# Performance work log

Hardware: AMD Instinct MI355X
Metric: run time of the kernel (lower is better)

Reference implementation:

```python
import jax, jax.numpy as jnp
import numpy as np

B, N, D, H = 4, 2048, 256, 4
DH = D // H
SS = DH ** -0.25  # sqrt(scale), applied to both qk0 and qk1
EPS = 1e-5


def _split_heads(t):
    # [B, N, D] -> [B, H, N, DH]
    b, n, _ = t.shape
    return t.reshape(b, n, H, DH).transpose(0, 2, 1, 3)


def _merge_heads(t):
    # [B, H, N, DH] -> [B, N, D]
    b, h, n, dh = t.shape
    return t.transpose(0, 2, 1, 3).reshape(b, n, h * dh)


def _layernorm(x, g, b):
    mu = jnp.mean(x, axis=-1, keepdims=True)
    var = jnp.mean(jnp.square(x - mu), axis=-1, keepdims=True)
    return (x - mu) * jax.lax.rsqrt(var + EPS) * g + b


def setup_inputs() -> dict:
    key = jax.random.key(0)
    ks = jax.random.split(key, 16)
    s = 0.02
    return {
        "x0": jax.random.normal(ks[0], (B, N, D), jnp.float32),
        "x1": jax.random.normal(ks[1], (B, N, D), jnp.float32),
        # weights stored as [in, out] (y = x @ W + b), matching torch Linear math
        "Wqk": jax.random.normal(ks[2], (D, D), jnp.float32) * s,
        "bqk": jnp.zeros((D,), jnp.float32),
        "Wv": jax.random.normal(ks[3], (D, D), jnp.float32) * s,
        "bv": jnp.zeros((D,), jnp.float32),
        "Wo": jax.random.normal(ks[4], (D, D), jnp.float32) * s,
        "bo": jnp.zeros((D,), jnp.float32),
        "W1": jax.random.normal(ks[5], (2 * D, 2 * D), jnp.float32) * s,
        "b1": jnp.zeros((2 * D,), jnp.float32),
        "ln_g": jnp.ones((2 * D,), jnp.float32),
        "ln_b": jnp.zeros((2 * D,), jnp.float32),
        "W2": jax.random.normal(ks[6], (2 * D, D), jnp.float32) * s,
        "b2": jnp.zeros((D,), jnp.float32),
    }


def reference(x0, x1, Wqk, bqk, Wv, bv, Wo, bo, W1, b1, ln_g, ln_b, W2, b2):
    qk0 = _split_heads(x0 @ Wqk + bqk) * SS  # [B,H,N,DH]
    qk1 = _split_heads(x1 @ Wqk + bqk) * SS
    v0 = _split_heads(x0 @ Wv + bv)
    v1 = _split_heads(x1 @ Wv + bv)

    # single shared similarity matrix, reused for both softmax directions
    sim = jnp.einsum("bhid,bhjd->bhij", qk0, qk1)  # [B,H,N0,N1]
    attn01 = jax.nn.softmax(sim, axis=-1)                      # rows over j
    attn10 = jax.nn.softmax(jnp.swapaxes(sim, -1, -2), axis=-1)  # rows over i

    m0 = jnp.einsum("bhij,bhjd->bhid", attn01, v1)  # [B,H,N0,DH]
    m1 = jnp.einsum("bhji,bhjd->bhid", jnp.swapaxes(attn10, -1, -2), v0)

    m0 = _merge_heads(m0) @ Wo + bo  # [B,N,D]
    m1 = _merge_heads(m1) @ Wo + bo

    def ffn(x, m):
        h = jnp.concatenate([x, m], axis=-1) @ W1 + b1
        h = jax.nn.gelu(_layernorm(h, ln_g, ln_b), approximate=False)
        return x + h @ W2 + b2

    return ffn(x0, m0), ffn(x1, m1)
```

## Files before the change

### kernel.cpp

```cpp
#include <hip/hip_runtime.h>
#include <hip/hip_bf16.h>
#include <math.h>

#define DEV static __device__ __forceinline__

typedef float f32x4 __attribute__((ext_vector_type(4)));
typedef short s16x8 __attribute__((ext_vector_type(8)));
typedef unsigned short u16;
typedef unsigned int u32;
typedef u32 u32x2 __attribute__((ext_vector_type(2)));
typedef u16 u16x4 __attribute__((ext_vector_type(4)));
typedef u16 u16x8 __attribute__((ext_vector_type(8)));

#define SSCALE 0.35355339059327379f

DEV f32x4 mfma16(s16x8 a, s16x8 b, f32x4 c) {
  return __builtin_amdgcn_mfma_f32_16x16x32_bf16(a, b, c, 0, 0, 0);
}

DEV float bf2f(u16 x) { u32 u = ((u32)x) << 16; float f; __builtin_memcpy(&f, &u, 4); return f; }
DEV u16 f2bf(float x) { __hip_bfloat16 b = __float2bfloat16(x); u16 r; __builtin_memcpy(&r, &b, 2); return r; }

DEV void gload_lds16(const void* g, void* l) {
  __builtin_amdgcn_global_load_lds((const __attribute__((address_space(1))) u32*)g,
                                   (__attribute__((address_space(3))) u32*)l, 16, 0, 0);
}

__global__ __launch_bounds__(256) void k_prep(
    const float* __restrict__ x0, const float* __restrict__ x1,
    const float* __restrict__ Wqk, const float* __restrict__ Wv,
    const float* __restrict__ Wo, const float* __restrict__ W1,
    const float* __restrict__ W2, const float* __restrict__ bo,
    const float* __restrict__ b1,
    u16* __restrict__ btqkv, u16* __restrict__ btF,
    u16* __restrict__ bt2, float* __restrict__ bc, u16* __restrict__ Xb)
{
  const int blk = blockIdx.x, tid = threadIdx.x;
  if (blk < 2048) {
    int idx = blk * 2048 + tid * 8;
    const float* src = (idx < 2097152) ? (x0 + idx) : (x1 + (idx - 2097152));
    f32x4 va = *(const f32x4*)src;
    f32x4 vb = *(const f32x4*)(src + 4);
    u16x8 o;
#pragma unroll
    for (int j = 0; j < 4; ++j) { o[j] = f2bf(va[j]); o[4 + j] = f2bf(vb[j]); }
    *(u16x8*)(Xb + idx) = o;
  } else if (blk < 2144) {
    __shared__ float T[64][65];
    int tb = blk - 2048;
    const float* src; u16* dst; int sld, dld, kr0, c0, drow0;
    if (tb < 16)      { src = Wqk; dst = btqkv; sld = 256; dld = 256; drow0 = 0;
                        kr0 = (tb >> 2) * 64; c0 = (tb & 3) * 64; }
    else if (tb < 32) { tb -= 16; src = Wv; dst = btqkv; sld = 256; dld = 256; drow0 = 256;
                        kr0 = (tb >> 2) * 64; c0 = (tb & 3) * 64; }
    else if (tb < 64) { tb -= 32; src = W1; dst = btF; sld = 512; dld = 512; drow0 = 0;
                        kr0 = (tb >> 3) * 64; c0 = (tb & 7) * 64; }
    else              { tb -= 64; src = W2; dst = bt2; sld = 256; dld = 512; drow0 = 0;
                        kr0 = (tb >> 2) * 64; c0 = (tb & 3) * 64; }
    int r = tid >> 2, cq = (tid & 3) * 16;
#pragma unroll
    for (int q = 0; q < 4; ++q) {
      f32x4 v = *(const f32x4*)(src + (size_t)(kr0 + r) * sld + c0 + cq + q * 4);
#pragma unroll
      for (int e = 0; e < 4; ++e) T[r][cq + q * 4 + e] = v[e];
    }
    __syncthreads();
    int c = tid >> 2, kq = (tid & 3) * 16;
#pragma unroll
    for (int q = 0; q < 2; ++q) {
      u16x8 o;
#pragma unroll
      for (int e = 0; e < 8; ++e) o[e] = f2bf(T[kq + q * 8 + e][c]);
      *(u16x8*)(dst + (size_t)(drow0 + c0 + c) * dld + kr0 + kq + q * 8) = o;
    }
  } else if (blk < 2656) {
    int wb = blk - 2144;
    int i = wb >> 1;
    int n = (wb & 1) * 256 + tid;
    float a0 = 0.f, a1 = 0.f, a2 = 0.f, a3 = 0.f;
    for (int j = 0; j < 256; j += 4) {
      a0 = fmaf(Wo[i * 256 + j],     W1[(size_t)(256 + j) * 512 + n], a0);
      a1 = fmaf(Wo[i * 256 + j + 1], W1[(size_t)(257 + j) * 512 + n], a1);
      a2 = fmaf(Wo[i * 256 + j + 2], W1[(size_t)(258 + j) * 512 + n], a2);
      a3 = fmaf(Wo[i * 256 + j + 3], W1[(size_t)(259 + j) * 512 + n], a3);
    }
    btF[(size_t)n * 512 + 256 + i] = f2bf((a0 + a1) + (a2 + a3));
  } else {
    int n = (blk - 2656) * 256 + tid;
    float acc = b1[n];
    for (int j = 0; j < 256; ++j)
      acc = fmaf(bo[j], W1[(size_t)(256 + j) * 512 + n], acc);
    bc[n] = acc;
  }
}

template <int KD, int K1, int EPI, int BN>
__global__ __launch_bounds__(256, 2) void k_gemm(
    const u16* __restrict__ A1, const u16* __restrict__ A2,
    const u16* __restrict__ Bt,
    const float* __restrict__ bias, const float* __restrict__ bias2,
    const float* __restrict__ res0, const float* __restrict__ res1,
    u16* __restrict__ outb, u16* __restrict__ outb2,
    float* __restrict__ outf, int Ncols)
{
  constexpr int MR = (BN == 128) ? 4 : 2;
  __shared__ char lds[16384 + 2 * BN * 64];
  char* ldsA = lds;
  char* ldsB = lds + 16384;
  const int tid = threadIdx.x;
  const int lane = tid & 63;
  const int w = tid >> 6;
  const int wm = (BN == 128) ? (w >> 1) : w;
  const int wn = (BN == 128) ? (w & 1) : 0;
  const int g = lane >> 4, li = lane & 15;
  const int m0 = blockIdx.x * 128, n0 = blockIdx.y * BN;

  auto stage = [&](int buf, int t) {
    const int k0 = t * 32;
#pragma unroll
    for (int it = 0; it < 2; ++it) {
      int chunk = it * 256 + w * 64 + lane;
      int row = chunk >> 2, c = chunk & 3;
      int kc = k0 + ((c ^ ((row >> 1) & 3)) << 3);
      const u16* src = (kc < K1) ? (A1 + (size_t)(m0 + row) * K1 + kc)
                                 : (A2 + (size_t)(m0 + row) * (KD - K1) + (kc - K1));
      gload_lds16(src, ldsA + buf * 8192 + (it * 256 + w * 64) * 16);
    }
#pragma unroll
    for (int it = 0; it < BN / 64; ++it) {
      int chunk = it * 256 + w * 64 + lane;
      int row = chunk >> 2, c = chunk & 3;
      int kc = k0 + ((c ^ ((row >> 1) & 3)) << 3);
      gload_lds16(Bt + (size_t)(n0 + row) * KD + kc,
                  ldsB + buf * (BN * 64) + (it * 256 + w * 64) * 16);
    }
  };

  f32x4 acc[MR][4] = {};

  stage(0, 0);
  __syncthreads();
  const int NT = KD / 32;
  for (int t = 0; t < NT; ++t) {
    if (t + 1 < NT) stage((t + 1) & 1, t + 1);
    const char* bufA = ldsA + (t & 1) * 8192;
    const char* bufB = ldsB + (t & 1) * (BN * 64);
    s16x8 af[MR], bfr[4];
#pragma unroll
    for (int rt = 0; rt < MR; ++rt) {
      int row = wm * (MR * 16) + rt * 16 + li;
      af[rt] = *(const s16x8*)(bufA + row * 64 + ((g ^ ((row >> 1) & 3)) << 4));
    }
#pragma unroll
    for (int ct = 0; ct < 4; ++ct) {
      int col = wn * 64 + ct * 16 + li;
      bfr[ct] = *(const s16x8*)(bufB + col * 64 + ((g ^ ((col >> 1) & 3)) << 4));
    }
#pragma unroll
    for (int rt = 0; rt < MR; ++rt)
#pragma unroll
      for (int ct = 0; ct < 4; ++ct)
        acc[rt][ct] = mfma16(af[rt], bfr[ct], acc[rt][ct]);
    __syncthreads();
  }

#pragma unroll
  for (int rt = 0; rt < MR; ++rt) {
#pragma unroll
    for (int ct = 0; ct < 4; ++ct) {
      const int growb = m0 + wm * (MR * 16) + rt * 16 + g * 4;
      const int gcol = n0 + wn * 64 + ct * 16 + li;
      if (EPI == 0) {
        const int dir = growb >> 13, bb = (growb >> 11) & 3, n = growb & 2047;
        if (gcol < 256) {
          const int h = gcol >> 6, dh = gcol & 63;
#pragma unroll
          for (int r = 0; r < 4; ++r) {
            float q = (acc[rt][ct][r] + bias[gcol]) * SSCALE;
            outb[((size_t)(dir * 16 + bb * 4 + h) * 2048 + (n + r)) * 64 + dh] = f2bf(q);
          }
        } else {
          const int c2 = gcol - 256, h = c2 >> 6, dh = c2 & 63;
          u16x4 pk;
#pragma unroll
          for (int r = 0; r < 4; ++r) pk[r] = f2bf(acc[rt][ct][r] + bias2[c2]);
          *(u16x4*)(outb2 + ((size_t)(dir * 16 + bb * 4 + h) * 64 + dh) * 2048 + n) = pk;
        }
      } else if (EPI == 1) {
#pragma unroll
        for (int r = 0; r < 4; ++r)
          outb[(size_t)(growb + r) * Ncols + gcol] = f2bf(acc[rt][ct][r] + bias[gcol]);
      } else {
#pragma unroll
        for (int r = 0; r < 4; ++r) {
          int grow = growb + r;
          float x = (grow < 8192) ? res0[(size_t)grow * 256 + gcol]
                                  : res1[(size_t)(grow - 8192) * 256 + gcol];
          outf[(size_t)grow * 256 + gcol] = acc[rt][ct][r] + bias[gcol] + x;
        }
      }
    }
  }
}

__global__ __launch_bounds__(256, 2) void k_attn(
    const u16* __restrict__ qk, const u16* __restrict__ vt, u16* __restrict__ m_all)
{
  __shared__ char Kl[2][8192];
  __shared__ char Vl[2][8192];
  const int tid = threadIdx.x, lane = tid & 63, w = tid >> 6;
  const int g = lane >> 4, li = lane & 15;
  const int sw = (blockIdx.x & 7) * 64 + (blockIdx.x >> 3);
  const int qblk = sw & 15;
  const int p = sw >> 4;
  const int dir = p >> 4, bh = p & 15;
  const char* Qg = (const char*)qk + (size_t)p * 262144;
  const char* Kg = (const char*)qk + (size_t)((dir ^ 1) * 16 + bh) * 262144;
  const char* Vg = (const char*)vt + (size_t)((dir ^ 1) * 16 + bh) * 262144;
  const int q0 = qblk * 128 + w * 32;
  const int perm = (li & 3) | ((li & 4) << 1) | ((li & 8) >> 1);

  s16x8 qf[2][2];
#pragma unroll
  for (int qt = 0; qt < 2; ++qt)
#pragma unroll
    for (int h = 0; h < 2; ++h)
      qf[qt][h] = *(const s16x8*)(Qg + (size_t)(q0 + qt * 16 + li) * 128 + h * 64 + g * 16);

  auto stageKV = [&](int buf, int jt) {
#pragma unroll
    for (int it = 0; it < 2; ++it) {
      int chunk = it * 256 + w * 64 + lane;
      int row = chunk >> 3, c = chunk & 7;
      int cc = (c ^ (row & 7)) << 4;
      gload_lds16(Kg + (size_t)(jt * 64 + row) * 128 + cc, &Kl[buf][(it * 256 + w * 64) * 16]);
    }
#pragma unroll
    for (int it = 0; it < 2; ++it) {
      int chunk = it * 256 + w * 64 + lane;
      int row = chunk >> 3, c = chunk & 7;
      int cc = (c ^ (row & 7)) << 4;
      gload_lds16(Vg + (size_t)row * 4096 + jt * 128 + cc, &Vl[buf][(it * 256 + w * 64) * 16]);
    }
  };

  f32x4 acco[2][4] = {};
  float accl[2] = {0.f, 0.f};

  stageKV(0, 0);
  __syncthreads();
  for (int jt = 0; jt < 32; ++jt) {
    if (jt + 1 < 32) stageKV((jt + 1) & 1, jt + 1);
    const char* Kb = Kl[jt & 1];
    const char* Vb = Vl[jt & 1];

    u32 pw[4][2][2];
#pragma unroll
    for (int kt = 0; kt < 4; ++kt) {
      const int krow = kt * 16 + perm;
      s16x8 kf0 = *(const s16x8*)(Kb + krow * 128 + ((g ^ (krow & 7)) << 4));
      s16x8 kf1 = *(const s16x8*)(Kb + krow * 128 + (((4 + g) ^ (krow & 7)) << 4));
#pragma unroll
      for (int qt = 0; qt < 2; ++qt) {
        f32x4 s = {0.f, 0.f, 0.f, 0.f};
        s = mfma16(kf0, qf[qt][0], s);
        s = mfma16(kf1, qf[qt][1], s);
        float p0 = __expf(s[0]), p1 = __expf(s[1]);
        float p2 = __expf(s[2]), p3 = __expf(s[3]);
        accl[qt] += (p0 + p1) + (p2 + p3);
        pw[kt][qt][0] = (u32)f2bf(p0) | ((u32)f2bf(p1) << 16);
        pw[kt][qt][1] = (u32)f2bf(p2) | ((u32)f2bf(p3) << 16);
      }
    }

    s16x8 pf[2][2];
#pragma unroll
    for (int ks = 0; ks < 2; ++ks)
#pragma unroll
      for (int qt = 0; qt < 2; ++qt) {
        u32 a0 = pw[ks * 2][qt][0], b0 = pw[ks * 2 + 1][qt][0];
        u32 a1 = pw[ks * 2][qt][1], b1 = pw[ks * 2 + 1][qt][1];
        asm("v_permlane32_swap_b32 %0, %1" : "+v"(a0), "+v"(b0));
        asm("v_permlane32_swap_b32 %0, %1" : "+v"(a1), "+v"(b1));
        u32 words[4] = {a0, a1, b0, b1};
        __builtin_memcpy(&pf[ks][qt], words, 16);
      }

#pragma unroll
    for (int ks = 0; ks < 2; ++ks)
#pragma unroll
      for (int dt = 0; dt < 4; ++dt) {
        const int vrow = dt * 16 + li;
        s16x8 vfr = *(const s16x8*)(Vb + vrow * 128 + (((ks * 4 + g) ^ (vrow & 7)) << 4));
        acco[0][dt] = mfma16(pf[ks][0], vfr, acco[0][dt]);
        acco[1][dt] = mfma16(pf[ks][1], vfr, acco[1][dt]);
      }
    __syncthreads();
  }

  float invq[2][4];
#pragma unroll
  for (int qt = 0; qt < 2; ++qt) {
    float v = accl[qt];
    v += __shfl_xor(v, 16);
    v += __shfl_xor(v, 32);
    float inv = 1.0f / v;
#pragma unroll
    for (int r = 0; r < 4; ++r) invq[qt][r] = __shfl(inv, g * 4 + r);
  }

  const int bb = bh >> 2, h = bh & 3;
#pragma unroll
  for (int qt = 0; qt < 2; ++qt) {
    const size_t rowb = (size_t)dir * 8192 + (size_t)bb * 2048 + q0 + qt * 16 + g * 4;
#pragma unroll
    for (int dt = 0; dt < 4; ++dt)
#pragma unroll
      for (int r = 0; r < 4; ++r)
        m_all[(rowb + r) * 256 + h * 64 + dt * 16 + li] = f2bf(acco[qt][dt][r] * invq[qt][r]);
  }
}

__global__ __launch_bounds__(256) void k_ln_gelu(
    const u16* __restrict__ h, const float* __restrict__ lg,
    const float* __restrict__ lb, u16* __restrict__ o)
{
  int lane = threadIdx.x & 63;
  size_t row = blockIdx.x * 4 + (threadIdx.x >> 6);
  s16x8 v = *(const s16x8*)(h + row * 512 + lane * 8);
  float f[8], s = 0.f, s2 = 0.f;
#pragma unroll
  for (int j = 0; j < 8; ++j) { f[j] = bf2f((u16)v[j]); s += f[j]; s2 += f[j] * f[j]; }
#pragma unroll
  for (int m = 1; m < 64; m <<= 1) { s += __shfl_xor(s, m); s2 += __shfl_xor(s2, m); }
  float mu = s * (1.0f / 512.0f);
  float var = s2 * (1.0f / 512.0f) - mu * mu;
  float rs = rsqrtf(var + 1e-5f);
  s16x8 ov;
#pragma unroll
  for (int j = 0; j < 8; ++j) {
    int c = lane * 8 + j;
    float y = (f[j] - mu) * rs * lg[c] + lb[c];
    float ge = 0.5f * y * (1.0f + erff(y * 0.70710678118654752f));
    ov[j] = (short)f2bf(ge);
  }
  *(s16x8*)(o + row * 512 + lane * 8) = ov;
}

extern "C" void kernel_launch(void* const* d_in, const int* in_sizes, int n_in,
                              void* d_out, int out_size, void* d_ws, size_t ws_size,
                              hipStream_t stream)
{
  const float* x0  = (const float*)d_in[0];
  const float* x1  = (const float*)d_in[1];
  const float* Wqk = (const float*)d_in[2];
  const float* bqk = (const float*)d_in[3];
  const float* Wv  = (const float*)d_in[4];
  const float* bv  = (const float*)d_in[5];
  const float* Wo  = (const float*)d_in[6];
  const float* bo  = (const float*)d_in[7];
  const float* W1  = (const float*)d_in[8];
  const float* b1  = (const float*)d_in[9];
  const float* lg  = (const float*)d_in[10];
  const float* lb  = (const float*)d_in[11];
  const float* W2  = (const float*)d_in[12];
  const float* b2  = (const float*)d_in[13];
  float* out = (float*)d_out;
  char* ws = (char*)d_ws;

  u16*   Xb    = (u16*)(ws + 0);
  u16*   qk    = (u16*)(ws + 8388608);
  u16*   vt    = (u16*)(ws + 16777216);
  u16*   m_all = (u16*)(ws + 25165824);
  u16*   hpre  = (u16*)(ws + 33554432);
  u16*   gact  = (u16*)(ws + 50331648);
  u16*   btqkv = (u16*)(ws + 67108864);
  u16*   btF   = (u16*)(ws + 67371008);
  u16*   bt2   = (u16*)(ws + 67895296);
  float* bc    = (float*)(ws + 68419584);

  k_prep<<<dim3(2658), dim3(256), 0, stream>>>(x0, x1, Wqk, Wv, Wo, W1, W2, bo, b1,
                                               btqkv, btF, bt2, bc, Xb);
  k_gemm<256, 256, 0, 128><<<dim3(128, 4), dim3(256), 0, stream>>>(
      Xb, nullptr, btqkv, bqk, bv, nullptr, nullptr, qk, vt, nullptr, 512);
  k_attn<<<dim3(512), dim3(256), 0, stream>>>(qk, vt, m_all);
  k_gemm<512, 256, 1, 128><<<dim3(128, 4), dim3(256), 0, stream>>>(
      Xb, m_all, btF, bc, nullptr, nullptr, nullptr, hpre, nullptr, nullptr, 512);
  k_ln_gelu<<<dim3(4096), dim3(256), 0, stream>>>(hpre, lg, lb, gact);
  k_gemm<512, 512, 3, 64><<<dim3(128, 4), dim3(256), 0, stream>>>(
      gact, nullptr, bt2, b2, nullptr, x0, x1, nullptr, nullptr, out, 256);
}
```

Baseline: 230.4 us.

## Split attention key range across two wave groups and fold log2e into scale

After: 223.4 us. 1.03x faster.

```diff
diff --git a/kernel.cpp b/kernel.cpp
--- a/kernel.cpp
+++ b/kernel.cpp
@@ -13,6 +13,7 @@
 typedef u16 u16x8 __attribute__((ext_vector_type(8)));
 
 #define SSCALE 0.35355339059327379f
+#define SS2 0.42466089345200966f
 
 DEV f32x4 mfma16(s16x8 a, s16x8 b, f32x4 c) {
   return __builtin_amdgcn_mfma_f32_16x16x32_bf16(a, b, c, 0, 0, 0);
@@ -20,6 +21,14 @@
 
 DEV float bf2f(u16 x) { u32 u = ((u32)x) << 16; float f; __builtin_memcpy(&f, &u, 4); return f; }
 DEV u16 f2bf(float x) { __hip_bfloat16 b = __float2bfloat16(x); u16 r; __builtin_memcpy(&r, &b, 2); return r; }
+
+DEV float fexp2(float x) {
+#if __has_builtin(__builtin_amdgcn_exp2f)
+  return __builtin_amdgcn_exp2f(x);
+#else
+  return exp2f(x);
+#endif
+}
 
 DEV void gload_lds16(const void* g, void* l) {
   __builtin_amdgcn_global_load_lds((const __attribute__((address_space(1))) u32*)g,
@@ -176,7 +185,7 @@
           const int h = gcol >> 6, dh = gcol & 63;
 #pragma unroll
           for (int r = 0; r < 4; ++r) {
-            float q = (acc[rt][ct][r] + bias[gcol]) * SSCALE;
+            float q = (acc[rt][ct][r] + bias[gcol]) * SS2;
             outb[((size_t)(dir * 16 + bb * 4 + h) * 2048 + (n + r)) * 64 + dh] = f2bf(q);
           }
         } else {
@@ -203,12 +212,13 @@
   }
 }
 
-__global__ __launch_bounds__(256, 2) void k_attn(
+__global__ __launch_bounds__(512, 4) void k_attn(
     const u16* __restrict__ qk, const u16* __restrict__ vt, u16* __restrict__ m_all)
 {
-  __shared__ char Kl[2][8192];
-  __shared__ char Vl[2][8192];
+  __shared__ char Kl[2][2][8192];
+  __shared__ char Vl[2][2][8192];
   const int tid = threadIdx.x, lane = tid & 63, w = tid >> 6;
+  const int half = w >> 2, wq = w & 3;
   const int g = lane >> 4, li = lane & 15;
   const int sw = (blockIdx.x & 7) * 64 + (blockIdx.x >> 3);
   const int qblk = sw & 15;
@@ -217,7 +227,7 @@
   const char* Qg = (const char*)qk + (size_t)p * 262144;
   const char* Kg = (const char*)qk + (size_t)((dir ^ 1) * 16 + bh) * 262144;
   const char* Vg = (const char*)vt + (size_t)((dir ^ 1) * 16 + bh) * 262144;
-  const int q0 = qblk * 128 + w * 32;
+  const int q0 = qblk * 128 + wq * 32;
   const int perm = (li & 3) | ((li & 4) << 1) | ((li & 8) >> 1);
 
   s16x8 qf[2][2];
@@ -228,19 +238,20 @@
       qf[qt][h] = *(const s16x8*)(Qg + (size_t)(q0 + qt * 16 + li) * 128 + h * 64 + g * 16);
 
   auto stageKV = [&](int buf, int jt) {
+    const int kb = half * 1024 + jt * 64;
 #pragma unroll
     for (int it = 0; it < 2; ++it) {
-      int chunk = it * 256 + w * 64 + lane;
+      int chunk = it * 256 + wq * 64 + lane;
       int row = chunk >> 3, c = chunk & 7;
       int cc = (c ^ (row & 7)) << 4;
-      gload_lds16(Kg + (size_t)(jt * 64 + row) * 128 + cc, &Kl[buf][(it * 256 + w * 64) * 16]);
+      gload_lds16(Kg + (size_t)(kb + row) * 128 + cc, &Kl[half][buf][chunk * 16]);
     }
 #pragma unroll
     for (int it = 0; it < 2; ++it) {
-      int chunk = it * 256 + w * 64 + lane;
+      int chunk = it * 256 + wq * 64 + lane;
       int row = chunk >> 3, c = chunk & 7;
       int cc = (c ^ (row & 7)) << 4;
-      gload_lds16(Vg + (size_t)row * 4096 + jt * 128 + cc, &Vl[buf][(it * 256 + w * 64) * 16]);
+      gload_lds16(Vg + (size_t)row * 4096 + kb * 2 + cc, &Vl[half][buf][chunk * 16]);
     }
   };
 
@@ -249,10 +260,10 @@
 
   stageKV(0, 0);
   __syncthreads();
-  for (int jt = 0; jt < 32; ++jt) {
-    if (jt + 1 < 32) stageKV((jt + 1) & 1, jt + 1);
-    const char* Kb = Kl[jt & 1];
-    const char* Vb = Vl[jt & 1];
+  for (int jt = 0; jt < 16; ++jt) {
+    if (jt + 1 < 16) stageKV((jt + 1) & 1, jt + 1);
+    const char* Kb = &Kl[half][jt & 1][0];
+    const char* Vb = &Vl[half][jt & 1][0];
 
     u32 pw[4][2][2];
 #pragma unroll
@@ -265,8 +276,8 @@
         f32x4 s = {0.f, 0.f, 0.f, 0.f};
         s = mfma16(kf0, qf[qt][0], s);
         s = mfma16(kf1, qf[qt][1], s);
-        float p0 = __expf(s[0]), p1 = __expf(s[1]);
-        float p2 = __expf(s[2]), p3 = __expf(s[3]);
+        float p0 = fexp2(s[0]), p1 = fexp2(s[1]);
+        float p2 = fexp2(s[2]), p3 = fexp2(s[3]);
         accl[qt] += (p0 + p1) + (p2 + p3);
         pw[kt][qt][0] = (u32)f2bf(p0) | ((u32)f2bf(p1) << 16);
         pw[kt][qt][1] = (u32)f2bf(p2) | ((u32)f2bf(p3) << 16);
@@ -298,26 +309,52 @@
     __syncthreads();
   }
 
-  float invq[2][4];
 #pragma unroll
   for (int qt = 0; qt < 2; ++qt) {
     float v = accl[qt];
     v += __shfl_xor(v, 16);
     v += __shfl_xor(v, 32);
-    float inv = 1.0f / v;
-#pragma unroll
-    for (int r = 0; r < 4; ++r) invq[qt][r] = __shfl(inv, g * 4 + r);
-  }
-
-  const int bb = bh >> 2, h = bh & 3;
-#pragma unroll
-  for (int qt = 0; qt < 2; ++qt) {
-    const size_t rowb = (size_t)dir * 8192 + (size_t)bb * 2048 + q0 + qt * 16 + g * 4;
-#pragma unroll
-    for (int dt = 0; dt < 4; ++dt)
-#pragma unroll
-      for (int r = 0; r < 4; ++r)
-        m_all[(rowb + r) * 256 + h * 64 + dt * 16 + li] = f2bf(acco[qt][dt][r] * invq[qt][r]);
+    accl[qt] = v;
+  }
+
+  float* scr  = (float*)&Kl[0][0][0];
+  float* lscr = (float*)&Vl[0][0][0];
+  if (half == 0) {
+#pragma unroll
+    for (int qt = 0; qt < 2; ++qt)
+#pragma unroll
+      for (int dt = 0; dt < 4; ++dt)
+        *(f32x4*)(scr + wq * 2048 + lane * 32 + (((qt * 4 + dt) * 4) ^ ((lane & 7) << 2))) =
+            acco[qt][dt];
+    if (lane < 16) {
+      lscr[wq * 32 + li] = accl[0];
+      lscr[wq * 32 + 16 + li] = accl[1];
+    }
+  }
+  __syncthreads();
+  if (half == 1) {
+    float invq[2][4];
+#pragma unroll
+    for (int qt = 0; qt < 2; ++qt) {
+      float ltot = accl[qt] + lscr[wq * 32 + qt * 16 + li];
+      float inv = 1.0f / ltot;
+#pragma unroll
+      for (int r = 0; r < 4; ++r) invq[qt][r] = __shfl(inv, g * 4 + r);
+    }
+    const int bb = bh >> 2, h = bh & 3;
+#pragma unroll
+    for (int qt = 0; qt < 2; ++qt) {
+      const size_t rowb = (size_t)dir * 8192 + (size_t)bb * 2048 + q0 + qt * 16 + g * 4;
+#pragma unroll
+      for (int dt = 0; dt < 4; ++dt) {
+        f32x4 o = *(const f32x4*)(scr + wq * 2048 + lane * 32 +
+                                  (((qt * 4 + dt) * 4) ^ ((lane & 7) << 2)));
+#pragma unroll
+        for (int r = 0; r < 4; ++r)
+          m_all[(rowb + r) * 256 + h * 64 + dt * 16 + li] =
+              f2bf((acco[qt][dt][r] + o[r]) * invq[qt][r]);
+      }
+    }
   }
 }
 
@@ -383,7 +420,7 @@
                                                btqkv, btF, bt2, bc, Xb);
   k_gemm<256, 256, 0, 128><<<dim3(128, 4), dim3(256), 0, stream>>>(
       Xb, nullptr, btqkv, bqk, bv, nullptr, nullptr, qk, vt, nullptr, 512);
-  k_attn<<<dim3(512), dim3(256), 0, stream>>>(qk, vt, m_all);
+  k_attn<<<dim3(512), dim3(512), 0, stream>>>(qk, vt, m_all);
   k_gemm<512, 256, 1, 128><<<dim3(128, 4), dim3(256), 0, stream>>>(
       Xb, m_all, btF, bc, nullptr, nullptr, nullptr, hpre, nullptr, nullptr, 512);
   k_ln_gelu<<<dim3(4096), dim3(256), 0, stream>>>(hpre, lg, lb, gact);
```
